# Performance work log

Measured on AMD Instinct MI355X. Metric: run time of the kernel, lower is better.

The kernel has to match this reference:

```python
import jax, jax.numpy as jnp
import numpy as np

TEMPERATURE = 0.05
EPS = 1e-6
N, D = 8192, 64


def setup_inputs() -> dict:
    key = jax.random.key(0)
    k1, k2 = jax.random.split(key)
    anchor_embeddings = jax.random.normal(k1, (N, D), dtype=jnp.float32)
    positive_embeddings = jax.random.normal(k2, (N, D), dtype=jnp.float32)
    return {"anchor_embeddings": anchor_embeddings,
            "positive_embeddings": positive_embeddings}


def _cos_matrix(x, y, nx, ny):
    # pairwise cosine sim with torch CosineSimilarity eps semantics:
    # dot / max(||x||*||y||, eps)
    return (x @ y.T) / jnp.maximum(nx[:, None] * ny[None, :], EPS)


def reference(anchor_embeddings, positive_embeddings):
    a, p = anchor_embeddings, positive_embeddings
    na = jnp.linalg.norm(a, axis=-1)  # [N]
    npn = jnp.linalg.norm(p, axis=-1)  # [N]

    inv_t = 1.0 / TEMPERATURE
    S_ap = _cos_matrix(a, p, na, npn)  # [N, N]
    S_aa = _cos_matrix(a, a, na, na)   # [N, N]
    S_pp = _cos_matrix(p, p, npn, npn)  # [N, N]

    E_ap = jnp.exp(S_ap * inv_t)
    E_aa = jnp.exp(S_aa * inv_t)
    E_pp = jnp.exp(S_pp * inv_t)

    self_term = jnp.exp(jnp.asarray(inv_t, dtype=a.dtype))  # exp(1/T)
    # partition_i = sum_j E_ap[i,j] + sum_j E_aa[i,j] - e^{1/T}
    #             + sum_j E_ap[j,i] + sum_j E_pp[j,i] - e^{1/T}
    partition = (E_ap.sum(axis=1) + E_aa.sum(axis=1)
                 + E_ap.sum(axis=0) + E_pp.sum(axis=0)
                 - 2.0 * self_term)

    # loss = -mean_i log( exp(cos(a_i,p_i)/T) / partition_i )
    pos_logit = jnp.diagonal(S_ap) * inv_t
    loss = -jnp.mean(pos_logit - jnp.log(partition))
    return loss
```

## Files before the change

kernel.cpp:

```cpp
#include <hip/hip_runtime.h>
#include <hip/hip_bf16.h>
#include <math.h>

#define N 8192
#define D 64
#define INVT 20.0f
#define EPS 1e-6f
#define ZSCALE 5.3715835f
#define NTILES 8256

typedef __attribute__((ext_vector_type(8))) short bf16x8;
typedef __attribute__((ext_vector_type(4))) float f32x4;

#if __has_builtin(__builtin_amdgcn_exp2f)
#define EXP2F(x) __builtin_amdgcn_exp2f(x)
#else
#define EXP2F(x) exp2f(x)
#endif


__device__ __forceinline__ void unrank(int t, int& bi, int& bj) {
    int b = (int)((257.0f - sqrtf(66049.0f - 8.0f * (float)t)) * 0.5f);
    while (b * (257 - b) / 2 > t) --b;
    while ((b + 1) * (256 - b) / 2 <= t) ++b;
    bi = b;
    bj = b + (t - b * (257 - b) / 2);
}

__global__ __launch_bounds__(256) void prep_kernel(
    const float* __restrict__ A, const float* __restrict__ P,
    __hip_bfloat16* __restrict__ Zn, float* __restrict__ diag20,
    float* __restrict__ lacc, unsigned* __restrict__ cnt) {
    if (blockIdx.x == 0 && threadIdx.x == 0) { *lacc = 0.0f; *cnt = 0u; }

    const int lane = threadIdx.x & 63;
    const int w    = threadIdx.x >> 6;
    const int r    = blockIdx.x * 4 + w;
    const int u    = lane >> 3, sub = lane & 7;
    const int upos = (u >> 2) * 64 + (u & 3) * 16;

    float a = A[r * D + lane];
    float p = P[r * D + lane];
    float sa = a * a, sp = p * p, dp = a * p;
    #pragma unroll
    for (int off = 1; off < 64; off <<= 1) {
        sa += __shfl_xor(sa, off, 64);
        sp += __shfl_xor(sp, off, 64);
        dp += __shfl_xor(dp, off, 64);
    }
    float na  = sqrtf(sa);
    float npn = sqrtf(sp);
    {
        int g = r >> 4, l2 = r & 15;
        Zn[(g * 128 + upos + l2) * 8 + sub] = __float2bfloat16(a * (ZSCALE / na));
    }
    {
        int R = N + r; int g = R >> 4, l2 = R & 15;
        Zn[(g * 128 + upos + l2) * 8 + sub] = __float2bfloat16(p * (ZSCALE / npn));
    }
    if (lane == 0)
        diag20[r] = (dp / fmaxf(na * npn, EPS)) * INVT;
}

__global__ __launch_bounds__(256, 4) void tiles_kernel(
    const __hip_bfloat16* __restrict__ Zn,
    float* __restrict__ rowbuf, float* __restrict__ colbuf) {
    __shared__ float rs[4][16][68];
    __shared__ float merged[2][128];
    __shared__ float cmerged[2][2][64];

    const int tid = threadIdx.x;
    const int lane = tid & 63, w = tid >> 6;
    const int wr = w >> 1, wc = w & 1;
    const int ln = lane & 15, q = lane >> 4;
    const bf16x8* Zf = (const bf16x8*)Zn;

    const int t0 = 2 * (int)blockIdx.x;
    const int t1 = t0 + 1;
    int bi0, bj0, bi1, bj1;
    unrank(t0, bi0, bj0);
    unrank(t1, bi1, bj1);

    const f32x4 zero = {0.0f, 0.0f, 0.0f, 0.0f};

    bf16x8 af0[4][2], bv0[4][2];
    #pragma unroll
    for (int ii = 0; ii < 4; ++ii) {
        int ga = bi0 * 8 + wr * 4 + ii;
        int gb = bj0 * 8 + wc * 4 + ii;
        #pragma unroll
        for (int kc = 0; kc < 2; ++kc) {
            af0[ii][kc] = Zf[ga * 128 + kc * 64 + lane];
            bv0[ii][kc] = Zf[gb * 128 + kc * 64 + lane];
        }
    }

    const bool dwave0 = (bi0 == bj0) && (wr == wc);
    float csum[4] = {0.0f, 0.0f, 0.0f, 0.0f};
    #pragma unroll
    for (int ii = 0; ii < 4; ++ii) {
        f32x4 acc[4];
        #pragma unroll
        for (int jj = 0; jj < 4; ++jj)
            acc[jj] = __builtin_amdgcn_mfma_f32_16x16x32_bf16(
                af0[ii][0], bv0[jj][0], zero, 0, 0, 0);
        #pragma unroll
        for (int jj = 0; jj < 4; ++jj)
            acc[jj] = __builtin_amdgcn_mfma_f32_16x16x32_bf16(
                af0[ii][1], bv0[jj][1], acc[jj], 0, 0, 0);

        f32x4 rsum_ii = {};
        #pragma unroll
        for (int jj = 0; jj < 4; ++jj) {
            f32x4 e;
            #pragma unroll
            for (int r = 0; r < 4; ++r) e[r] = EXP2F(acc[jj][r]);
            if (dwave0 && (ii == jj)) {
                #pragma unroll
                for (int r = 0; r < 4; ++r)
                    if (ln == q * 4 + r) e[r] = 0.0f;
            }
            rsum_ii += e;
            csum[jj] += (e[0] + e[1]) + (e[2] + e[3]);
        }
        *(f32x4*)&rs[w][ln][ii * 16 + q * 4] = rsum_ii;
    }

    bf16x8 af1[4][2], bv1[4][2];
    #pragma unroll
    for (int ii = 0; ii < 4; ++ii) {
        int ga = bi1 * 8 + wr * 4 + ii;
        int gb = bj1 * 8 + wc * 4 + ii;
        #pragma unroll
        for (int kc = 0; kc < 2; ++kc) {
            af1[ii][kc] = Zf[ga * 128 + kc * 64 + lane];
            bv1[ii][kc] = Zf[gb * 128 + kc * 64 + lane];
        }
    }

    {
        float rowsum = 0.0f;
        #pragma unroll
        for (int l = 0; l < 16; ++l) rowsum += rs[w][l][lane];
        merged[wc][wr * 64 + lane] = rowsum;

        float cs0 = csum[0], cs1 = csum[1], cs2 = csum[2], cs3 = csum[3];
        cs0 += __shfl_xor(cs0, 16, 64); cs0 += __shfl_xor(cs0, 32, 64);
        cs1 += __shfl_xor(cs1, 16, 64); cs1 += __shfl_xor(cs1, 32, 64);
        cs2 += __shfl_xor(cs2, 16, 64); cs2 += __shfl_xor(cs2, 32, 64);
        cs3 += __shfl_xor(cs3, 16, 64); cs3 += __shfl_xor(cs3, 32, 64);
        float cval = (q == 0) ? cs0 : (q == 1) ? cs1 : (q == 2) ? cs2 : cs3;
        cmerged[wr][wc][q * 16 + ln] = cval;
        __syncthreads();

        if (tid < 128) {
            rowbuf[t0 * 128 + tid] = merged[0][tid] + merged[1][tid];
        } else if (bi0 != bj0) {
            int col = tid - 128;
            colbuf[t0 * 128 + col] =
                cmerged[0][col >> 6][col & 63] + cmerged[1][col >> 6][col & 63];
        }
    }
    __syncthreads();

    const bool dwave1 = (bi1 == bj1) && (wr == wc);
    float csumB[4] = {0.0f, 0.0f, 0.0f, 0.0f};
    #pragma unroll
    for (int ii = 0; ii < 4; ++ii) {
        f32x4 acc[4];
        #pragma unroll
        for (int jj = 0; jj < 4; ++jj)
            acc[jj] = __builtin_amdgcn_mfma_f32_16x16x32_bf16(
                af1[ii][0], bv1[jj][0], zero, 0, 0, 0);
        #pragma unroll
        for (int jj = 0; jj < 4; ++jj)
            acc[jj] = __builtin_amdgcn_mfma_f32_16x16x32_bf16(
                af1[ii][1], bv1[jj][1], acc[jj], 0, 0, 0);

        f32x4 rsum_ii = {};
        #pragma unroll
        for (int jj = 0; jj < 4; ++jj) {
            f32x4 e;
            #pragma unroll
            for (int r = 0; r < 4; ++r) e[r] = EXP2F(acc[jj][r]);
            if (dwave1 && (ii == jj)) {
                #pragma unroll
                for (int r = 0; r < 4; ++r)
                    if (ln == q * 4 + r) e[r] = 0.0f;
            }
            rsum_ii += e;
            csumB[jj] += (e[0] + e[1]) + (e[2] + e[3]);
        }
        *(f32x4*)&rs[w][ln][ii * 16 + q * 4] = rsum_ii;
    }

    {
        float rowsum = 0.0f;
        #pragma unroll
        for (int l = 0; l < 16; ++l) rowsum += rs[w][l][lane];
        merged[wc][wr * 64 + lane] = rowsum;

        float cs0 = csumB[0], cs1 = csumB[1], cs2 = csumB[2], cs3 = csumB[3];
        cs0 += __shfl_xor(cs0, 16, 64); cs0 += __shfl_xor(cs0, 32, 64);
        cs1 += __shfl_xor(cs1, 16, 64); cs1 += __shfl_xor(cs1, 32, 64);
        cs2 += __shfl_xor(cs2, 16, 64); cs2 += __shfl_xor(cs2, 32, 64);
        cs3 += __shfl_xor(cs3, 16, 64); cs3 += __shfl_xor(cs3, 32, 64);
        float cval = (q == 0) ? cs0 : (q == 1) ? cs1 : (q == 2) ? cs2 : cs3;
        cmerged[wr][wc][q * 16 + ln] = cval;
        __syncthreads();

        if (tid < 128) {
            rowbuf[t1 * 128 + tid] = merged[0][tid] + merged[1][tid];
        } else if (bi1 != bj1) {
            int col = tid - 128;
            colbuf[t1 * 128 + col] =
                cmerged[0][col >> 6][col & 63] + cmerged[1][col >> 6][col & 63];
        }
    }
}

__global__ __launch_bounds__(256) void reduce_kernel(
    const float* __restrict__ rowbuf, const float* __restrict__ colbuf,
    float* __restrict__ part) {
    const int R  = (int)blockIdx.x * 256 + (int)threadIdx.x;
    const int bi = R >> 7, c = R & 127;
    const int base = bi * (257 - bi) / 2;

    float s = 0.0f;
    const int nrow = 128 - bi;
    #pragma unroll 4
    for (int k = 0; k < nrow; ++k)
        s += rowbuf[(base + k) * 128 + c];
    #pragma unroll 4
    for (int r = 0; r < bi; ++r)
        s += colbuf[(r * (257 - r) / 2 + (bi - r)) * 128 + c];
    part[R] = s;
}

__global__ __launch_bounds__(256) void loss_kernel(
    const float* __restrict__ part, const float* __restrict__ diag20,
    float* __restrict__ lacc, unsigned* __restrict__ cnt, float* __restrict__ out) {
    int i = blockIdx.x * 256 + threadIdx.x;
    float v = logf(part[i] + part[N + i]) - diag20[i];
    #pragma unroll
    for (int off = 32; off > 0; off >>= 1) v += __shfl_down(v, off, 64);
    __shared__ float wsm[4];
    int lane = threadIdx.x & 63, wv = threadIdx.x >> 6;
    if (lane == 0) wsm[wv] = v;
    __syncthreads();
    if (threadIdx.x == 0) {
        atomicAdd(lacc, wsm[0] + wsm[1] + wsm[2] + wsm[3]);
        __threadfence();
        unsigned old = atomicAdd(cnt, 1u);
        if (old == (N / 256 - 1)) {
            float tot = atomicAdd(lacc, 0.0f);
            out[0] = tot * (1.0f / (float)N);
        }
    }
}

extern "C" void kernel_launch(void* const* d_in, const int* in_sizes, int n_in,
                              void* d_out, int out_size, void* d_ws, size_t ws_size,
                              hipStream_t stream) {
    const float* A = (const float*)d_in[0];
    const float* P = (const float*)d_in[1];

    __hip_bfloat16* Zn = (__hip_bfloat16*)d_ws;
    float* diag20 = (float*)((char*)d_ws + 2u * N * D * sizeof(__hip_bfloat16));
    float* rowbuf = diag20 + N;
    float* colbuf = rowbuf + NTILES * 128;
    float* part   = colbuf + NTILES * 128;
    float* lacc   = part + 2 * N;
    unsigned* cnt = (unsigned*)(lacc + 1);

    prep_kernel<<<N / 4, 256, 0, stream>>>(A, P, Zn, diag20, lacc, cnt);

    tiles_kernel<<<NTILES / 2, 256, 0, stream>>>(Zn, rowbuf, colbuf);

    reduce_kernel<<<2 * N / 256, 256, 0, stream>>>(rowbuf, colbuf, part);

    loss_kernel<<<N / 256, 256, 0, stream>>>(part, diag20, lacc, cnt, (float*)d_out);
}
```

Measured before the change: 107.5 us.

## Reuse anchor fragments across tile pair, move barrier, split reduce across waves

```diff
diff --git a/kernel.cpp b/kernel.cpp
--- a/kernel.cpp
+++ b/kernel.cpp
@@ -129,12 +129,24 @@
     bf16x8 af1[4][2], bv1[4][2];
     #pragma unroll
     for (int ii = 0; ii < 4; ++ii) {
-        int ga = bi1 * 8 + wr * 4 + ii;
         int gb = bj1 * 8 + wc * 4 + ii;
         #pragma unroll
-        for (int kc = 0; kc < 2; ++kc) {
-            af1[ii][kc] = Zf[ga * 128 + kc * 64 + lane];
+        for (int kc = 0; kc < 2; ++kc)
             bv1[ii][kc] = Zf[gb * 128 + kc * 64 + lane];
+    }
+    if (bi1 == bi0) {
+        #pragma unroll
+        for (int ii = 0; ii < 4; ++ii) {
+            af1[ii][0] = af0[ii][0];
+            af1[ii][1] = af0[ii][1];
+        }
+    } else {
+        #pragma unroll
+        for (int ii = 0; ii < 4; ++ii) {
+            int ga = bi1 * 8 + wr * 4 + ii;
+            #pragma unroll
+            for (int kc = 0; kc < 2; ++kc)
+                af1[ii][kc] = Zf[ga * 128 + kc * 64 + lane];
         }
     }
 
@@ -161,7 +173,6 @@
                 cmerged[0][col >> 6][col & 63] + cmerged[1][col >> 6][col & 63];
         }
     }
-    __syncthreads();
 
     const bool dwave1 = (bi1 == bj1) && (wr == wc);
     float csumB[4] = {0.0f, 0.0f, 0.0f, 0.0f};
@@ -194,6 +205,8 @@
         *(f32x4*)&rs[w][ln][ii * 16 + q * 4] = rsum_ii;
     }
 
+    __syncthreads();
+
     {
         float rowsum = 0.0f;
         #pragma unroll
@@ -220,21 +233,33 @@
 }
 
 __global__ __launch_bounds__(256) void reduce_kernel(
-    const float* __restrict__ rowbuf, const float* __restrict__ colbuf,
-    float* __restrict__ part) {
-    const int R  = (int)blockIdx.x * 256 + (int)threadIdx.x;
-    const int bi = R >> 7, c = R & 127;
+    const float* __restrict__ rowbuf, float* __restrict__ part) {
+    __shared__ float red[4][64];
+    const int b    = (int)blockIdx.x;
+    const int bi   = b >> 1;
+    const int cb   = (b & 1) * 64;
+    const int ci   = (int)threadIdx.x & 63;
+    const int h    = (int)threadIdx.x >> 6;
+    const int c    = cb + ci;
+    const int nrow = 128 - bi;
     const int base = bi * (257 - bi) / 2;
 
     float s = 0.0f;
-    const int nrow = 128 - bi;
-    #pragma unroll 4
-    for (int k = 0; k < nrow; ++k)
-        s += rowbuf[(base + k) * 128 + c];
-    #pragma unroll 4
-    for (int r = 0; r < bi; ++r)
-        s += colbuf[(r * (257 - r) / 2 + (bi - r)) * 128 + c];
-    part[R] = s;
+    #pragma unroll 8
+    for (int k = h * 32; k < h * 32 + 32; ++k) {
+        int t;
+        if (k < nrow) {
+            t = base + k;
+        } else {
+            int r = k - nrow;
+            t = NTILES + r * (257 - r) / 2 + (bi - r);
+        }
+        s += rowbuf[t * 128 + c];
+    }
+    red[h][ci] = s;
+    __syncthreads();
+    if (h == 0)
+        part[bi * 128 + c] = red[0][ci] + red[1][ci] + red[2][ci] + red[3][ci];
 }
 
 __global__ __launch_bounds__(256) void loss_kernel(
@@ -277,7 +302,7 @@
 
     tiles_kernel<<<NTILES / 2, 256, 0, stream>>>(Zn, rowbuf, colbuf);
 
-    reduce_kernel<<<2 * N / 256, 256, 0, stream>>>(rowbuf, colbuf, part);
+    reduce_kernel<<<256, 256, 0, stream>>>(rowbuf, part);
 
     loss_kernel<<<N / 256, 256, 0, stream>>>(part, diag20, lacc, cnt, (float*)d_out);
 }
```

Measured after the change: 101.1 us. 1.06x faster.
